# Kernel tuning notes

Hardware: AMD Instinct MI355X
Metric: run time of the kernel (lower is better)

## Reference

```python
import jax, jax.numpy as jnp
import numpy as np

N_NODES = 50000
N_EDGES = 600000
N_GRAPHS = 512
LN_EPS = 1e-5


def setup_inputs() -> dict:
    key = jax.random.key(0)
    ks = jax.random.split(key, 18)
    s = 0.05
    return {
        "x": jax.random.normal(ks[0], (N_NODES, 29), jnp.float32),
        "xdims": jax.random.normal(ks[1], (N_NODES, 3), jnp.float32),
        "xsttype": jax.random.randint(ks[2], (N_NODES,), 0, 256),
        "edge_index": jax.random.randint(ks[3], (2, N_EDGES), 0, N_NODES),
        "batch": jnp.sort(jax.random.randint(ks[4], (N_NODES,), 0, N_GRAPHS)),
        "st_emb": jax.random.normal(ks[5], (256, 12), jnp.float32) * s,
        "Wl1": jax.random.normal(ks[6], (128, 44), jnp.float32) * s,
        "bl1": jnp.zeros((128,), jnp.float32),
        "Wr1": jax.random.normal(ks[7], (128, 44), jnp.float32) * s,
        "g1": jnp.ones((128,), jnp.float32),
        "beta1": jnp.zeros((128,), jnp.float32),
        "Wl2": jax.random.normal(ks[8], (128, 128), jnp.float32) * s,
        "bl2": jnp.zeros((128,), jnp.float32),
        "Wr2": jax.random.normal(ks[9], (128, 128), jnp.float32) * s,
        "g2": jnp.ones((128,), jnp.float32),
        "beta2": jnp.zeros((128,), jnp.float32),
        "Wlin": jax.random.normal(ks[10], (10, 256), jnp.float32) * s,
        "blin": jnp.zeros((10,), jnp.float32),
    }


def layernorm(h, g, b):
    mu = jnp.mean(h, axis=-1, keepdims=True)
    var = jnp.mean(jnp.square(h - mu), axis=-1, keepdims=True)
    return g * (h - mu) * jax.lax.rsqrt(var + LN_EPS) + b


def sage_conv(h, src, dst, Wl, bl, Wr):
    # PyG SAGEConv: lin_l(mean_j x_j) + lin_r(x_i); messages flow src -> dst.
    msg = h[src]                                            # [E, D]
    agg = jax.ops.segment_sum(msg, dst, num_segments=N_NODES)
    cnt = jax.ops.segment_sum(jnp.ones((msg.shape[0],), h.dtype), dst, num_segments=N_NODES)
    mean = agg / jnp.maximum(cnt, 1.0)[:, None]
    return mean @ Wl.T + bl + h @ Wr.T


def reference(x, xdims, xsttype, edge_index, batch, st_emb,
              Wl1, bl1, Wr1, g1, beta1,
              Wl2, bl2, Wr2, g2, beta2,
              Wlin, blin):
    src, dst = edge_index[0], edge_index[1]
    h = jnp.concatenate([x, xdims, st_emb[xsttype]], axis=1)   # [N, 44]
    # Layer 1
    h = jax.nn.relu(layernorm(sage_conv(h, src, dst, Wl1, bl1, Wr1), g1, beta1))
    # Layer 2
    h = jax.nn.relu(layernorm(sage_conv(h, src, dst, Wl2, bl2, Wr2), g2, beta2))
    # dropout inactive (inference)
    hs = jax.ops.segment_sum(h, batch, num_segments=N_GRAPHS)
    nc = jax.ops.segment_sum(jnp.ones((h.shape[0],), h.dtype), batch, num_segments=N_GRAPHS)
    hmean = hs / jnp.maximum(nc, 1.0)[:, None]
    hmax = jax.ops.segment_max(h, batch, num_segments=N_GRAPHS)
    pooled = jnp.concatenate([hmean, hmax], axis=1)            # [G, 256]
    return pooled @ Wlin.T + blin                              # [G, 10]
```

## Files before the change

kernel.cpp:

```cpp
#include <hip/hip_runtime.h>
#include <hip/hip_bf16.h>
#include <math.h>

#define N_NODES 50000
#define N_EDGES 600000
#define N_GRAPHS 512
#define LN_EPS 1e-5f
#define CAP 96
#define EDGE_BLOCKS ((N_EDGES / 4 + 255) / 256)
#define PREP_BLOCKS ((N_NODES * 48 + 255) / 256)

typedef short bf16x8 __attribute__((ext_vector_type(8)));
typedef float f32x4 __attribute__((ext_vector_type(4)));

__device__ __forceinline__ unsigned short f2bf(float f) {
    unsigned int x = __float_as_uint(f);
    return (unsigned short)((x + 0x7fffu + ((x >> 16) & 1u)) >> 16);
}
__device__ __forceinline__ float bflo(unsigned int u) { return __uint_as_float(u << 16); }
__device__ __forceinline__ float bfhi(unsigned int u) { return __uint_as_float(u & 0xffff0000u); }

__global__ __launch_bounds__(256) void zero_kernel(int* __restrict__ cnt)
{
    int i = blockIdx.x * 256 + threadIdx.x;
    if (i < N_NODES) cnt[i] = 0;
}

__global__ __launch_bounds__(256) void prep_fill_kernel(
    const float* __restrict__ x, const float* __restrict__ xdims,
    const int* __restrict__ stt, const float* __restrict__ st_emb,
    const float* __restrict__ Wl1, const float* __restrict__ Wr1,
    const float* __restrict__ Wl2, const float* __restrict__ Wr2,
    const int* __restrict__ batch,
    const int* __restrict__ esrc_in, const int* __restrict__ edst_in,
    unsigned short* __restrict__ Xc1, unsigned short* __restrict__ Wc1,
    unsigned short* __restrict__ Wc2, int* __restrict__ cnt,
    int* __restrict__ esrc_pad, int* __restrict__ starts)
{
    if (blockIdx.x < EDGE_BLOCKS) {
        int t = blockIdx.x * 256 + threadIdx.x;
        int e4 = t * 4;
        if (e4 < N_EDGES) {
            int4 d4 = *(const int4*)(edst_in + e4);
            int4 s4 = *(const int4*)(esrc_in + e4);
            int sl0 = atomicAdd(&cnt[d4.x], 1);
            int sl1 = atomicAdd(&cnt[d4.y], 1);
            int sl2 = atomicAdd(&cnt[d4.z], 1);
            int sl3 = atomicAdd(&cnt[d4.w], 1);
            if (sl0 < CAP) esrc_pad[(size_t)d4.x * CAP + sl0] = s4.x;
            if (sl1 < CAP) esrc_pad[(size_t)d4.y * CAP + sl1] = s4.y;
            if (sl2 < CAP) esrc_pad[(size_t)d4.z * CAP + sl2] = s4.z;
            if (sl3 < CAP) esrc_pad[(size_t)d4.w * CAP + sl3] = s4.w;
        }
        return;
    }
    int idx = (blockIdx.x - EDGE_BLOCKS) * 256 + threadIdx.x;

    if (idx < N_NODES * 48) {
        int n = idx / 48;
        int c = idx - n * 48;
        float v;
        if (c < 29)       v = x[n * 29 + c];
        else if (c < 32)  v = xdims[n * 3 + (c - 29)];
        else if (c < 44)  v = st_emb[stt[n] * 12 + (c - 32)];
        else              v = 0.f;
        Xc1[(size_t)n * 96 + c] = f2bf(v);
    }
    if (idx < 128 * 96) {
        int f = idx / 96, k = idx - f * 96;
        float v;
        if (k < 44)       v = Wr1[f * 44 + k];
        else if (k < 48)  v = 0.f;
        else if (k < 92)  v = Wl1[f * 44 + (k - 48)];
        else              v = 0.f;
        Wc1[idx] = f2bf(v);
    }
    if (idx < 128 * 256) {
        int f = idx >> 8, k = idx & 255;
        float v = (k < 128) ? Wr2[f * 128 + k] : Wl2[f * 128 + (k - 128)];
        Wc2[idx] = f2bf(v);
    }
    if (idx < N_NODES) {
        int b = batch[idx];
        int pb = (idx == 0) ? -1 : batch[idx - 1];
        for (int g = pb + 1; g <= b; ++g) starts[g] = idx;
        if (idx == N_NODES - 1)
            for (int g = b + 1; g <= N_GRAPHS; ++g) starts[g] = N_NODES;
    }
}

__global__ __launch_bounds__(256) void agg1_kernel(const int* __restrict__ cnt,
                                                   const int* __restrict__ esrc_pad,
                                                   unsigned short* __restrict__ Xc)
{
    int n = blockIdx.x * 4 + (threadIdx.x >> 6);
    if (n >= N_NODES) return;
    const int lane = threadIdx.x & 63;
    const int grp = lane >> 3;
    const int sl  = lane & 7;
    const int slc = (sl < 5) ? sl : 5;
    int degT = cnt[n];
    int deg  = (degT < CAP) ? degT : CAP;
    int er = esrc_pad[(size_t)n * CAP + lane];
    float a0=0.f,a1=0.f,a2=0.f,a3=0.f,a4=0.f,a5=0.f,a6=0.f,a7=0.f;
    const uint4* base = (const uint4*)Xc;
    const int c1 = deg - 1;
    int lim = (deg < 64) ? deg : 64;
    for (int e = 0; e < lim; e += 16) {
        int eA = e + grp, eB = eA + 8;
        int sA = __shfl(er, (eA < c1) ? eA : c1);
        int sB = __shfl(er, (eB < c1) ? eB : c1);
        uint4 va = base[(size_t)sA * 12 + slc];
        uint4 vb = base[(size_t)sB * 12 + slc];
        float mA = (eA < deg) ? 1.f : 0.f;
        float mB = (eB < deg) ? 1.f : 0.f;
        a0 += mA * bflo(va.x) + mB * bflo(vb.x);
        a1 += mA * bfhi(va.x) + mB * bfhi(vb.x);
        a2 += mA * bflo(va.y) + mB * bflo(vb.y);
        a3 += mA * bfhi(va.y) + mB * bfhi(vb.y);
        a4 += mA * bflo(va.z) + mB * bflo(vb.z);
        a5 += mA * bfhi(va.z) + mB * bfhi(vb.z);
        a6 += mA * bflo(va.w) + mB * bflo(vb.w);
        a7 += mA * bfhi(va.w) + mB * bfhi(vb.w);
    }
    for (int e = 64; e < deg; e += 16) {
        int eA = e + grp, eB = eA + 8;
        int sA = esrc_pad[(size_t)n * CAP + ((eA < c1) ? eA : c1)];
        int sB = esrc_pad[(size_t)n * CAP + ((eB < c1) ? eB : c1)];
        uint4 va = base[(size_t)sA * 12 + slc];
        uint4 vb = base[(size_t)sB * 12 + slc];
        float mA = (eA < deg) ? 1.f : 0.f;
        float mB = (eB < deg) ? 1.f : 0.f;
        a0 += mA * bflo(va.x) + mB * bflo(vb.x);
        a1 += mA * bfhi(va.x) + mB * bfhi(vb.x);
        a2 += mA * bflo(va.y) + mB * bflo(vb.y);
        a3 += mA * bfhi(va.y) + mB * bfhi(vb.y);
        a4 += mA * bflo(va.z) + mB * bflo(vb.z);
        a5 += mA * bfhi(va.z) + mB * bfhi(vb.z);
        a6 += mA * bflo(va.w) + mB * bflo(vb.w);
        a7 += mA * bfhi(va.w) + mB * bfhi(vb.w);
    }
    #pragma unroll
    for (int m = 8; m <= 32; m <<= 1) {
        a0 += __shfl_xor(a0, m); a1 += __shfl_xor(a1, m);
        a2 += __shfl_xor(a2, m); a3 += __shfl_xor(a3, m);
        a4 += __shfl_xor(a4, m); a5 += __shfl_xor(a5, m);
        a6 += __shfl_xor(a6, m); a7 += __shfl_xor(a7, m);
    }
    if (grp == 0 && sl < 6) {
        float inv = (degT > 0) ? 1.f / (float)degT : 0.f;
        uint4 p;
        p.x = (unsigned int)f2bf(a0 * inv) | ((unsigned int)f2bf(a1 * inv) << 16);
        p.y = (unsigned int)f2bf(a2 * inv) | ((unsigned int)f2bf(a3 * inv) << 16);
        p.z = (unsigned int)f2bf(a4 * inv) | ((unsigned int)f2bf(a5 * inv) << 16);
        p.w = (unsigned int)f2bf(a6 * inv) | ((unsigned int)f2bf(a7 * inv) << 16);
        ((uint4*)Xc)[(size_t)n * 12 + 6 + sl] = p;
    }
}

__global__ __launch_bounds__(256) void agg2_kernel(const int* __restrict__ cnt,
                                                   const int* __restrict__ esrc_pad,
                                                   unsigned short* __restrict__ Xc)
{
    int n = blockIdx.x * 4 + (threadIdx.x >> 6);
    if (n >= N_NODES) return;
    const int lane = threadIdx.x & 63;
    const int grp = lane >> 4;
    const int sl  = lane & 15;
    int degT = cnt[n];
    int deg  = (degT < CAP) ? degT : CAP;
    int er = esrc_pad[(size_t)n * CAP + lane];
    float a0=0.f,a1=0.f,a2=0.f,a3=0.f,a4=0.f,a5=0.f,a6=0.f,a7=0.f;
    const uint4* base = (const uint4*)Xc;
    const int c1 = deg - 1;
    int lim = (deg < 64) ? deg : 64;
    for (int e = 0; e < lim; e += 16) {
        int eA = e + grp, eB = eA + 4, eC = eA + 8, eD = eA + 12;
        int sA = __shfl(er, (eA < c1) ? eA : c1);
        int sB = __shfl(er, (eB < c1) ? eB : c1);
        int sC = __shfl(er, (eC < c1) ? eC : c1);
        int sD = __shfl(er, (eD < c1) ? eD : c1);
        uint4 va = base[(size_t)sA * 32 + sl];
        uint4 vb = base[(size_t)sB * 32 + sl];
        uint4 vc = base[(size_t)sC * 32 + sl];
        uint4 vd = base[(size_t)sD * 32 + sl];
        float mA = (eA < deg) ? 1.f : 0.f;
        float mB = (eB < deg) ? 1.f : 0.f;
        float mC = (eC < deg) ? 1.f : 0.f;
        float mD = (eD < deg) ? 1.f : 0.f;
        a0 += mA * bflo(va.x) + mB * bflo(vb.x) + mC * bflo(vc.x) + mD * bflo(vd.x);
        a1 += mA * bfhi(va.x) + mB * bfhi(vb.x) + mC * bfhi(vc.x) + mD * bfhi(vd.x);
        a2 += mA * bflo(va.y) + mB * bflo(vb.y) + mC * bflo(vc.y) + mD * bflo(vd.y);
        a3 += mA * bfhi(va.y) + mB * bfhi(vb.y) + mC * bfhi(vc.y) + mD * bfhi(vd.y);
        a4 += mA * bflo(va.z) + mB * bflo(vb.z) + mC * bflo(vc.z) + mD * bflo(vd.z);
        a5 += mA * bfhi(va.z) + mB * bfhi(vb.z) + mC * bfhi(vc.z) + mD * bfhi(vd.z);
        a6 += mA * bflo(va.w) + mB * bflo(vb.w) + mC * bflo(vc.w) + mD * bflo(vd.w);
        a7 += mA * bfhi(va.w) + mB * bfhi(vb.w) + mC * bfhi(vc.w) + mD * bfhi(vd.w);
    }
    for (int e = 64; e < deg; e += 16) {
        int eA = e + grp, eB = eA + 4, eC = eA + 8, eD = eA + 12;
        int sA = esrc_pad[(size_t)n * CAP + ((eA < c1) ? eA : c1)];
        int sB = esrc_pad[(size_t)n * CAP + ((eB < c1) ? eB : c1)];
        int sC = esrc_pad[(size_t)n * CAP + ((eC < c1) ? eC : c1)];
        int sD = esrc_pad[(size_t)n * CAP + ((eD < c1) ? eD : c1)];
        uint4 va = base[(size_t)sA * 32 + sl];
        uint4 vb = base[(size_t)sB * 32 + sl];
        uint4 vc = base[(size_t)sC * 32 + sl];
        uint4 vd = base[(size_t)sD * 32 + sl];
        float mA = (eA < deg) ? 1.f : 0.f;
        float mB = (eB < deg) ? 1.f : 0.f;
        float mC = (eC < deg) ? 1.f : 0.f;
        float mD = (eD < deg) ? 1.f : 0.f;
        a0 += mA * bflo(va.x) + mB * bflo(vb.x) + mC * bflo(vc.x) + mD * bflo(vd.x);
        a1 += mA * bfhi(va.x) + mB * bfhi(vb.x) + mC * bfhi(vc.x) + mD * bfhi(vd.x);
        a2 += mA * bflo(va.y) + mB * bflo(vb.y) + mC * bflo(vc.y) + mD * bflo(vd.y);
        a3 += mA * bfhi(va.y) + mB * bfhi(vb.y) + mC * bfhi(vc.y) + mD * bfhi(vd.y);
        a4 += mA * bflo(va.z) + mB * bflo(vb.z) + mC * bflo(vc.z) + mD * bflo(vd.z);
        a5 += mA * bfhi(va.z) + mB * bfhi(vb.z) + mC * bfhi(vc.z) + mD * bfhi(vd.z);
        a6 += mA * bflo(va.w) + mB * bflo(vb.w) + mC * bflo(vc.w) + mD * bflo(vd.w);
        a7 += mA * bfhi(va.w) + mB * bfhi(vb.w) + mC * bfhi(vc.w) + mD * bfhi(vd.w);
    }
    #pragma unroll
    for (int m = 16; m <= 32; m <<= 1) {
        a0 += __shfl_xor(a0, m); a1 += __shfl_xor(a1, m);
        a2 += __shfl_xor(a2, m); a3 += __shfl_xor(a3, m);
        a4 += __shfl_xor(a4, m); a5 += __shfl_xor(a5, m);
        a6 += __shfl_xor(a6, m); a7 += __shfl_xor(a7, m);
    }
    if (grp == 0) {
        float inv = (degT > 0) ? 1.f / (float)degT : 0.f;
        uint4 p;
        p.x = (unsigned int)f2bf(a0 * inv) | ((unsigned int)f2bf(a1 * inv) << 16);
        p.y = (unsigned int)f2bf(a2 * inv) | ((unsigned int)f2bf(a3 * inv) << 16);
        p.z = (unsigned int)f2bf(a4 * inv) | ((unsigned int)f2bf(a5 * inv) << 16);
        p.w = (unsigned int)f2bf(a6 * inv) | ((unsigned int)f2bf(a7 * inv) << 16);
        ((uint4*)Xc)[(size_t)n * 32 + 16 + sl] = p;
    }
}

template <int KPAD>
__global__ __launch_bounds__(256) void mfma_layer_kernel(
    const unsigned short* __restrict__ X, const unsigned short* __restrict__ W,
    const float* __restrict__ bl, const float* __restrict__ g,
    const float* __restrict__ beta,
    unsigned short* __restrict__ Out, int outStride)
{
    const int lane = threadIdx.x & 63;
    const int wv   = threadIdx.x >> 6;
    const int l15  = lane & 15;
    const int l4   = lane >> 4;
    const int row0 = blockIdx.x * 128 + wv * 32;

    int rA0 = row0 + l15;       if (rA0 > N_NODES - 1) rA0 = N_NODES - 1;
    int rA1 = row0 + 16 + l15;  if (rA1 > N_NODES - 1) rA1 = N_NODES - 1;

    f32x4 acc[2][8];
    #pragma unroll
    for (int m = 0; m < 2; ++m)
        #pragma unroll
        for (int n = 0; n < 8; ++n) acc[m][n] = (f32x4){0.f, 0.f, 0.f, 0.f};

    const int kb = l4 * 8;
    #pragma unroll
    for (int ks = 0; ks < KPAD / 32; ++ks) {
        const int k = ks * 32 + kb;
        bf16x8 a0 = *(const bf16x8*)(X + (size_t)rA0 * KPAD + k);
        bf16x8 a1 = *(const bf16x8*)(X + (size_t)rA1 * KPAD + k);
        #pragma unroll
        for (int ni = 0; ni < 8; ++ni) {
            bf16x8 b = *(const bf16x8*)(W + (size_t)(ni * 16 + l15) * KPAD + k);
            acc[0][ni] = __builtin_amdgcn_mfma_f32_16x16x32_bf16(a0, b, acc[0][ni], 0, 0, 0);
            acc[1][ni] = __builtin_amdgcn_mfma_f32_16x16x32_bf16(a1, b, acc[1][ni], 0, 0, 0);
        }
    }

    float blv[8], gv[8], bev[8];
    #pragma unroll
    for (int ni = 0; ni < 8; ++ni) {
        int f = ni * 16 + l15;
        blv[ni] = bl[f]; gv[ni] = g[f]; bev[ni] = beta[f];
    }

    #pragma unroll
    for (int mi = 0; mi < 2; ++mi) {
        #pragma unroll
        for (int r = 0; r < 4; ++r) {
            float v[8];
            float s1 = 0.f, s2 = 0.f;
            #pragma unroll
            for (int ni = 0; ni < 8; ++ni) {
                float t = acc[mi][ni][r] + blv[ni];
                v[ni] = t; s1 += t; s2 += t * t;
            }
            #pragma unroll
            for (int m = 8; m >= 1; m >>= 1) {
                s1 += __shfl_xor(s1, m);
                s2 += __shfl_xor(s2, m);
            }
            float mu   = s1 * (1.f / 128.f);
            float var  = s2 * (1.f / 128.f) - mu * mu;
            float rstd = rsqrtf(var + LN_EPS);
            int node = row0 + mi * 16 + l4 * 4 + r;
            if (node < N_NODES) {
                #pragma unroll
                for (int ni = 0; ni < 8; ++ni) {
                    float o = gv[ni] * (v[ni] - mu) * rstd + bev[ni];
                    o = fmaxf(o, 0.f);
                    Out[(size_t)node * outStride + ni * 16 + l15] = f2bf(o);
                }
            }
        }
    }
}

__global__ __launch_bounds__(256) void poolhead_kernel(const unsigned short* __restrict__ h2,
                                                       const int* __restrict__ starts,
                                                       const float* __restrict__ Wlin,
                                                       const float* __restrict__ blin,
                                                       float* __restrict__ out)
{
    const int g  = blockIdx.x;
    const int j2 = threadIdx.x & 63;
    const int h  = threadIdx.x >> 6;
    const int s0 = starts[g], s1 = starts[g + 1];
    float sa = 0.f, sb = 0.f, ma = -INFINITY, mb = -INFINITY;
    const unsigned int* base = (const unsigned int*)h2;
    int n = s0 + h;
    for (; n + 4 < s1; n += 8) {
        unsigned int u0 = base[(size_t)n * 64 + j2];
        unsigned int u1 = base[(size_t)(n + 4) * 64 + j2];
        float l0 = bflo(u0), h0 = bfhi(u0);
        float l1 = bflo(u1), h1 = bfhi(u1);
        sa += l0 + l1; sb += h0 + h1;
        ma = fmaxf(ma, fmaxf(l0, l1));
        mb = fmaxf(mb, fmaxf(h0, h1));
    }
    if (n < s1) {
        unsigned int u = base[(size_t)n * 64 + j2];
        float lo = bflo(u), hi = bfhi(u);
        sa += lo; sb += hi;
        ma = fmaxf(ma, lo); mb = fmaxf(mb, hi);
    }
    __shared__ float red[4][4][64];
    __shared__ float pooled[256];
    red[h][0][j2] = sa; red[h][1][j2] = sb; red[h][2][j2] = ma; red[h][3][j2] = mb;
    __syncthreads();
    if (h == 0) {
        #pragma unroll
        for (int o = 1; o < 4; ++o) {
            sa += red[o][0][j2]; sb += red[o][1][j2];
            ma = fmaxf(ma, red[o][2][j2]); mb = fmaxf(mb, red[o][3][j2]);
        }
        int c = s1 - s0;
        float inv = (c > 0) ? 1.f / (float)c : 0.f;
        pooled[2 * j2]           = sa * inv;
        pooled[2 * j2 + 1]       = sb * inv;
        pooled[128 + 2 * j2]     = (c > 0) ? ma : 0.f;
        pooled[128 + 2 * j2 + 1] = (c > 0) ? mb : 0.f;
    }
    __syncthreads();
    if (threadIdx.x < 10) {
        const float* w = Wlin + threadIdx.x * 256;
        float acc = blin[threadIdx.x];
        for (int k = 0; k < 256; ++k) acc += pooled[k] * w[k];
        out[g * 10 + threadIdx.x] = acc;
    }
}

extern "C" void kernel_launch(void* const* d_in, const int* in_sizes, int n_in,
                              void* d_out, int out_size, void* d_ws, size_t ws_size,
                              hipStream_t stream)
{
    const float* x      = (const float*)d_in[0];
    const float* xdims  = (const float*)d_in[1];
    const int*   stt    = (const int*)d_in[2];
    const int*   eidx   = (const int*)d_in[3];
    const int*   batch  = (const int*)d_in[4];
    const float* st_emb = (const float*)d_in[5];
    const float* Wl1 = (const float*)d_in[6];
    const float* bl1 = (const float*)d_in[7];
    const float* Wr1 = (const float*)d_in[8];
    const float* g1  = (const float*)d_in[9];
    const float* be1 = (const float*)d_in[10];
    const float* Wl2 = (const float*)d_in[11];
    const float* bl2 = (const float*)d_in[12];
    const float* Wr2 = (const float*)d_in[13];
    const float* g2  = (const float*)d_in[14];
    const float* be2 = (const float*)d_in[15];
    const float* Wlin = (const float*)d_in[16];
    const float* blin = (const float*)d_in[17];
    float* out = (float*)d_out;

    const int* esrc_in = eidx;
    const int* edst_in = eidx + N_EDGES;

    char* ws = (char*)d_ws;
    size_t o = 0;
    auto carve = [&](size_t bytes) { void* p = ws + o; o = (o + bytes + 255) & ~(size_t)255; return p; };
    unsigned short* Xc1  = (unsigned short*)carve((size_t)N_NODES * 96 * 2);
    unsigned short* Xc2  = (unsigned short*)carve((size_t)N_NODES * 256 * 2);
    unsigned short* h2bf = (unsigned short*)carve((size_t)N_NODES * 128 * 2);
    unsigned short* Wc1  = (unsigned short*)carve((size_t)128 * 96 * 2);
    unsigned short* Wc2  = (unsigned short*)carve((size_t)128 * 256 * 2);
    int*   cnt      = (int*)carve((size_t)N_NODES * 4);
    int*   esrc_pad = (int*)carve((size_t)N_NODES * CAP * 4);
    int*   starts   = (int*)carve((size_t)(N_GRAPHS + 1) * 4);
    (void)ws_size;

    zero_kernel<<<(N_NODES + 255) / 256, 256, 0, stream>>>(cnt);

    prep_fill_kernel<<<EDGE_BLOCKS + PREP_BLOCKS, 256, 0, stream>>>(
        x, xdims, stt, st_emb, Wl1, Wr1, Wl2, Wr2, batch,
        esrc_in, edst_in, Xc1, Wc1, Wc2, cnt, esrc_pad, starts);

    agg1_kernel<<<(N_NODES + 3) / 4, 256, 0, stream>>>(cnt, esrc_pad, Xc1);
    mfma_layer_kernel<96><<<(N_NODES + 127) / 128, 256, 0, stream>>>(
        Xc1, Wc1, bl1, g1, be1, Xc2, 256);

    agg2_kernel<<<(N_NODES + 3) / 4, 256, 0, stream>>>(cnt, esrc_pad, Xc2);
    mfma_layer_kernel<256><<<(N_NODES + 127) / 128, 256, 0, stream>>>(
        Xc2, Wc2, bl2, g2, be2, h2bf, 128);

    poolhead_kernel<<<N_GRAPHS, 256, 0, stream>>>(h2bf, starts, Wlin, blin, out);
}
```

Measured before the change: 130.8 us.

## Fuse neighbor mean aggregation into MFMA layer kernels with 16-bit adjacency

Each layer's separate gather-mean kernel is removed. Each wave now aggregates neighbor features for its 16 nodes into LDS, then runs the MFMA GEMM with LayerNorm and ReLU, reading the self half from global memory and the mean half from shared memory. This drops two launches and the global write and re-read of the aggregated features. The adjacency list shrinks to 16-bit indices with a 64-slot cap, and node feature buffers hold only the self half. In exchange, each wave aggregates its 16 nodes one after another, which may hide gather latency less well, and any node with more than 64 in-edges has the extra edges dropped from its sum.

```diff
diff --git a/kernel.cpp b/kernel.cpp
--- a/kernel.cpp
+++ b/kernel.cpp
@@ -6,9 +6,9 @@
 #define N_EDGES 600000
 #define N_GRAPHS 512
 #define LN_EPS 1e-5f
-#define CAP 96
+#define CAP 64
 #define EDGE_BLOCKS ((N_EDGES / 4 + 255) / 256)
-#define PREP_BLOCKS ((N_NODES * 48 + 255) / 256)
+#define PREP_BLOCKS ((N_NODES * 64 + 255) / 256)
 
 typedef short bf16x8 __attribute__((ext_vector_type(8)));
 typedef float f32x4 __attribute__((ext_vector_type(4)));
@@ -33,9 +33,9 @@
     const float* __restrict__ Wl2, const float* __restrict__ Wr2,
     const int* __restrict__ batch,
     const int* __restrict__ esrc_in, const int* __restrict__ edst_in,
-    unsigned short* __restrict__ Xc1, unsigned short* __restrict__ Wc1,
+    unsigned short* __restrict__ Xh1, unsigned short* __restrict__ Wc1,
     unsigned short* __restrict__ Wc2, int* __restrict__ cnt,
-    int* __restrict__ esrc_pad, int* __restrict__ starts)
+    unsigned short* __restrict__ adj, int* __restrict__ starts)
 {
     if (blockIdx.x < EDGE_BLOCKS) {
         int t = blockIdx.x * 256 + threadIdx.x;
@@ -47,32 +47,32 @@
             int sl1 = atomicAdd(&cnt[d4.y], 1);
             int sl2 = atomicAdd(&cnt[d4.z], 1);
             int sl3 = atomicAdd(&cnt[d4.w], 1);
-            if (sl0 < CAP) esrc_pad[(size_t)d4.x * CAP + sl0] = s4.x;
-            if (sl1 < CAP) esrc_pad[(size_t)d4.y * CAP + sl1] = s4.y;
-            if (sl2 < CAP) esrc_pad[(size_t)d4.z * CAP + sl2] = s4.z;
-            if (sl3 < CAP) esrc_pad[(size_t)d4.w * CAP + sl3] = s4.w;
+            if (sl0 < CAP) adj[(size_t)d4.x * CAP + sl0] = (unsigned short)s4.x;
+            if (sl1 < CAP) adj[(size_t)d4.y * CAP + sl1] = (unsigned short)s4.y;
+            if (sl2 < CAP) adj[(size_t)d4.z * CAP + sl2] = (unsigned short)s4.z;
+            if (sl3 < CAP) adj[(size_t)d4.w * CAP + sl3] = (unsigned short)s4.w;
         }
         return;
     }
     int idx = (blockIdx.x - EDGE_BLOCKS) * 256 + threadIdx.x;
 
-    if (idx < N_NODES * 48) {
-        int n = idx / 48;
-        int c = idx - n * 48;
+    if (idx < N_NODES * 64) {
+        int n = idx >> 6;
+        int c = idx & 63;
         float v;
         if (c < 29)       v = x[n * 29 + c];
         else if (c < 32)  v = xdims[n * 3 + (c - 29)];
         else if (c < 44)  v = st_emb[stt[n] * 12 + (c - 32)];
         else              v = 0.f;
-        Xc1[(size_t)n * 96 + c] = f2bf(v);
-    }
-    if (idx < 128 * 96) {
-        int f = idx / 96, k = idx - f * 96;
+        Xh1[idx] = f2bf(v);
+    }
+    if (idx < 128 * 128) {
+        int f = idx >> 7, k = idx & 127;
         float v;
-        if (k < 44)       v = Wr1[f * 44 + k];
-        else if (k < 48)  v = 0.f;
-        else if (k < 92)  v = Wl1[f * 44 + (k - 48)];
-        else              v = 0.f;
+        if (k < 44)        v = Wr1[f * 44 + k];
+        else if (k < 64)   v = 0.f;
+        else if (k < 108)  v = Wl1[f * 44 + (k - 64)];
+        else               v = 0.f;
         Wc1[idx] = f2bf(v);
     }
     if (idx < 128 * 256) {
@@ -89,188 +89,97 @@
     }
 }
 
-__global__ __launch_bounds__(256) void agg1_kernel(const int* __restrict__ cnt,
-                                                   const int* __restrict__ esrc_pad,
-                                                   unsigned short* __restrict__ Xc)
-{
-    int n = blockIdx.x * 4 + (threadIdx.x >> 6);
-    if (n >= N_NODES) return;
-    const int lane = threadIdx.x & 63;
-    const int grp = lane >> 3;
-    const int sl  = lane & 7;
-    const int slc = (sl < 5) ? sl : 5;
-    int degT = cnt[n];
-    int deg  = (degT < CAP) ? degT : CAP;
-    int er = esrc_pad[(size_t)n * CAP + lane];
-    float a0=0.f,a1=0.f,a2=0.f,a3=0.f,a4=0.f,a5=0.f,a6=0.f,a7=0.f;
-    const uint4* base = (const uint4*)Xc;
-    const int c1 = deg - 1;
-    int lim = (deg < 64) ? deg : 64;
-    for (int e = 0; e < lim; e += 16) {
-        int eA = e + grp, eB = eA + 8;
-        int sA = __shfl(er, (eA < c1) ? eA : c1);
-        int sB = __shfl(er, (eB < c1) ? eB : c1);
-        uint4 va = base[(size_t)sA * 12 + slc];
-        uint4 vb = base[(size_t)sB * 12 + slc];
-        float mA = (eA < deg) ? 1.f : 0.f;
-        float mB = (eB < deg) ? 1.f : 0.f;
-        a0 += mA * bflo(va.x) + mB * bflo(vb.x);
-        a1 += mA * bfhi(va.x) + mB * bfhi(vb.x);
-        a2 += mA * bflo(va.y) + mB * bflo(vb.y);
-        a3 += mA * bfhi(va.y) + mB * bfhi(vb.y);
-        a4 += mA * bflo(va.z) + mB * bflo(vb.z);
-        a5 += mA * bfhi(va.z) + mB * bfhi(vb.z);
-        a6 += mA * bflo(va.w) + mB * bflo(vb.w);
-        a7 += mA * bfhi(va.w) + mB * bfhi(vb.w);
-    }
-    for (int e = 64; e < deg; e += 16) {
-        int eA = e + grp, eB = eA + 8;
-        int sA = esrc_pad[(size_t)n * CAP + ((eA < c1) ? eA : c1)];
-        int sB = esrc_pad[(size_t)n * CAP + ((eB < c1) ? eB : c1)];
-        uint4 va = base[(size_t)sA * 12 + slc];
-        uint4 vb = base[(size_t)sB * 12 + slc];
-        float mA = (eA < deg) ? 1.f : 0.f;
-        float mB = (eB < deg) ? 1.f : 0.f;
-        a0 += mA * bflo(va.x) + mB * bflo(vb.x);
-        a1 += mA * bfhi(va.x) + mB * bfhi(vb.x);
-        a2 += mA * bflo(va.y) + mB * bflo(vb.y);
-        a3 += mA * bfhi(va.y) + mB * bfhi(vb.y);
-        a4 += mA * bflo(va.z) + mB * bflo(vb.z);
-        a5 += mA * bfhi(va.z) + mB * bfhi(vb.z);
-        a6 += mA * bflo(va.w) + mB * bflo(vb.w);
-        a7 += mA * bfhi(va.w) + mB * bfhi(vb.w);
-    }
-    #pragma unroll
-    for (int m = 8; m <= 32; m <<= 1) {
-        a0 += __shfl_xor(a0, m); a1 += __shfl_xor(a1, m);
-        a2 += __shfl_xor(a2, m); a3 += __shfl_xor(a3, m);
-        a4 += __shfl_xor(a4, m); a5 += __shfl_xor(a5, m);
-        a6 += __shfl_xor(a6, m); a7 += __shfl_xor(a7, m);
-    }
-    if (grp == 0 && sl < 6) {
-        float inv = (degT > 0) ? 1.f / (float)degT : 0.f;
-        uint4 p;
-        p.x = (unsigned int)f2bf(a0 * inv) | ((unsigned int)f2bf(a1 * inv) << 16);
-        p.y = (unsigned int)f2bf(a2 * inv) | ((unsigned int)f2bf(a3 * inv) << 16);
-        p.z = (unsigned int)f2bf(a4 * inv) | ((unsigned int)f2bf(a5 * inv) << 16);
-        p.w = (unsigned int)f2bf(a6 * inv) | ((unsigned int)f2bf(a7 * inv) << 16);
-        ((uint4*)Xc)[(size_t)n * 12 + 6 + sl] = p;
-    }
-}
-
-__global__ __launch_bounds__(256) void agg2_kernel(const int* __restrict__ cnt,
-                                                   const int* __restrict__ esrc_pad,
-                                                   unsigned short* __restrict__ Xc)
-{
-    int n = blockIdx.x * 4 + (threadIdx.x >> 6);
-    if (n >= N_NODES) return;
-    const int lane = threadIdx.x & 63;
-    const int grp = lane >> 4;
-    const int sl  = lane & 15;
-    int degT = cnt[n];
-    int deg  = (degT < CAP) ? degT : CAP;
-    int er = esrc_pad[(size_t)n * CAP + lane];
-    float a0=0.f,a1=0.f,a2=0.f,a3=0.f,a4=0.f,a5=0.f,a6=0.f,a7=0.f;
-    const uint4* base = (const uint4*)Xc;
-    const int c1 = deg - 1;
-    int lim = (deg < 64) ? deg : 64;
-    for (int e = 0; e < lim; e += 16) {
-        int eA = e + grp, eB = eA + 4, eC = eA + 8, eD = eA + 12;
-        int sA = __shfl(er, (eA < c1) ? eA : c1);
-        int sB = __shfl(er, (eB < c1) ? eB : c1);
-        int sC = __shfl(er, (eC < c1) ? eC : c1);
-        int sD = __shfl(er, (eD < c1) ? eD : c1);
-        uint4 va = base[(size_t)sA * 32 + sl];
-        uint4 vb = base[(size_t)sB * 32 + sl];
-        uint4 vc = base[(size_t)sC * 32 + sl];
-        uint4 vd = base[(size_t)sD * 32 + sl];
-        float mA = (eA < deg) ? 1.f : 0.f;
-        float mB = (eB < deg) ? 1.f : 0.f;
-        float mC = (eC < deg) ? 1.f : 0.f;
-        float mD = (eD < deg) ? 1.f : 0.f;
-        a0 += mA * bflo(va.x) + mB * bflo(vb.x) + mC * bflo(vc.x) + mD * bflo(vd.x);
-        a1 += mA * bfhi(va.x) + mB * bfhi(vb.x) + mC * bfhi(vc.x) + mD * bfhi(vd.x);
-        a2 += mA * bflo(va.y) + mB * bflo(vb.y) + mC * bflo(vc.y) + mD * bflo(vd.y);
-        a3 += mA * bfhi(va.y) + mB * bfhi(vb.y) + mC * bfhi(vc.y) + mD * bfhi(vd.y);
-        a4 += mA * bflo(va.z) + mB * bflo(vb.z) + mC * bflo(vc.z) + mD * bflo(vd.z);
-        a5 += mA * bfhi(va.z) + mB * bfhi(vb.z) + mC * bfhi(vc.z) + mD * bfhi(vd.z);
-        a6 += mA * bflo(va.w) + mB * bflo(vb.w) + mC * bflo(vc.w) + mD * bflo(vd.w);
-        a7 += mA * bfhi(va.w) + mB * bfhi(vb.w) + mC * bfhi(vc.w) + mD * bfhi(vd.w);
-    }
-    for (int e = 64; e < deg; e += 16) {
-        int eA = e + grp, eB = eA + 4, eC = eA + 8, eD = eA + 12;
-        int sA = esrc_pad[(size_t)n * CAP + ((eA < c1) ? eA : c1)];
-        int sB = esrc_pad[(size_t)n * CAP + ((eB < c1) ? eB : c1)];
-        int sC = esrc_pad[(size_t)n * CAP + ((eC < c1) ? eC : c1)];
-        int sD = esrc_pad[(size_t)n * CAP + ((eD < c1) ? eD : c1)];
-        uint4 va = base[(size_t)sA * 32 + sl];
-        uint4 vb = base[(size_t)sB * 32 + sl];
-        uint4 vc = base[(size_t)sC * 32 + sl];
-        uint4 vd = base[(size_t)sD * 32 + sl];
-        float mA = (eA < deg) ? 1.f : 0.f;
-        float mB = (eB < deg) ? 1.f : 0.f;
-        float mC = (eC < deg) ? 1.f : 0.f;
-        float mD = (eD < deg) ? 1.f : 0.f;
-        a0 += mA * bflo(va.x) + mB * bflo(vb.x) + mC * bflo(vc.x) + mD * bflo(vd.x);
-        a1 += mA * bfhi(va.x) + mB * bfhi(vb.x) + mC * bfhi(vc.x) + mD * bfhi(vd.x);
-        a2 += mA * bflo(va.y) + mB * bflo(vb.y) + mC * bflo(vc.y) + mD * bflo(vd.y);
-        a3 += mA * bfhi(va.y) + mB * bfhi(vb.y) + mC * bfhi(vc.y) + mD * bfhi(vd.y);
-        a4 += mA * bflo(va.z) + mB * bflo(vb.z) + mC * bflo(vc.z) + mD * bflo(vd.z);
-        a5 += mA * bfhi(va.z) + mB * bfhi(vb.z) + mC * bfhi(vc.z) + mD * bfhi(vd.z);
-        a6 += mA * bflo(va.w) + mB * bflo(vb.w) + mC * bflo(vc.w) + mD * bflo(vd.w);
-        a7 += mA * bfhi(va.w) + mB * bfhi(vb.w) + mC * bfhi(vc.w) + mD * bfhi(vd.w);
-    }
-    #pragma unroll
-    for (int m = 16; m <= 32; m <<= 1) {
-        a0 += __shfl_xor(a0, m); a1 += __shfl_xor(a1, m);
-        a2 += __shfl_xor(a2, m); a3 += __shfl_xor(a3, m);
-        a4 += __shfl_xor(a4, m); a5 += __shfl_xor(a5, m);
-        a6 += __shfl_xor(a6, m); a7 += __shfl_xor(a7, m);
-    }
-    if (grp == 0) {
-        float inv = (degT > 0) ? 1.f / (float)degT : 0.f;
-        uint4 p;
-        p.x = (unsigned int)f2bf(a0 * inv) | ((unsigned int)f2bf(a1 * inv) << 16);
-        p.y = (unsigned int)f2bf(a2 * inv) | ((unsigned int)f2bf(a3 * inv) << 16);
-        p.z = (unsigned int)f2bf(a4 * inv) | ((unsigned int)f2bf(a5 * inv) << 16);
-        p.w = (unsigned int)f2bf(a6 * inv) | ((unsigned int)f2bf(a7 * inv) << 16);
-        ((uint4*)Xc)[(size_t)n * 32 + 16 + sl] = p;
-    }
-}
-
 template <int KPAD>
-__global__ __launch_bounds__(256) void mfma_layer_kernel(
-    const unsigned short* __restrict__ X, const unsigned short* __restrict__ W,
+__global__ __launch_bounds__(256) void fused_layer_kernel(
+    const int* __restrict__ cnt, const unsigned short* __restrict__ adj,
+    const unsigned short* __restrict__ Xh,
+    const unsigned short* __restrict__ W,
     const float* __restrict__ bl, const float* __restrict__ g,
     const float* __restrict__ beta,
-    unsigned short* __restrict__ Out, int outStride)
-{
-    const int lane = threadIdx.x & 63;
-    const int wv   = threadIdx.x >> 6;
-    const int l15  = lane & 15;
-    const int l4   = lane >> 4;
-    const int row0 = blockIdx.x * 128 + wv * 32;
-
-    int rA0 = row0 + l15;       if (rA0 > N_NODES - 1) rA0 = N_NODES - 1;
-    int rA1 = row0 + 16 + l15;  if (rA1 > N_NODES - 1) rA1 = N_NODES - 1;
-
-    f32x4 acc[2][8];
+    unsigned short* __restrict__ Out)
+{
+    constexpr int DHALF = KPAD / 2;
+    constexpr int CH  = DHALF / 8;
+    constexpr int NG  = 64 / CH;
+    constexpr int NL  = 16 / NG;
+    constexpr int RSU = CH + 1;
+    __shared__ uint4 smean[64 * RSU];
+
+    const int lane  = threadIdx.x & 63;
+    const int wv    = threadIdx.x >> 6;
+    const int nbase = blockIdx.x * 64 + wv * 16;
+
+    {
+        const int grp = lane / CH;
+        const int sl  = lane % CH;
+        const uint4* gbase = (const uint4*)Xh;
+        for (int i = 0; i < 16; ++i) {
+            int n = nbase + i;
+            if (n >= N_NODES) break;
+            int degT = cnt[n];
+            int deg  = (degT < CAP) ? degT : CAP;
+            int er = adj[(size_t)n * CAP + lane];
+            float a0=0.f,a1=0.f,a2=0.f,a3=0.f,a4=0.f,a5=0.f,a6=0.f,a7=0.f;
+            const int c1 = deg - 1;
+            for (int e = 0; e < deg; e += 16) {
+                uint4 v[NL]; float mk[NL];
+                #pragma unroll
+                for (int j = 0; j < NL; ++j) {
+                    int ee = e + j * NG + grp;
+                    int s = __shfl(er, (ee < c1) ? ee : c1);
+                    v[j]  = gbase[(size_t)s * CH + sl];
+                    mk[j] = (ee < deg) ? 1.f : 0.f;
+                }
+                #pragma unroll
+                for (int j = 0; j < NL; ++j) {
+                    a0 += mk[j] * bflo(v[j].x); a1 += mk[j] * bfhi(v[j].x);
+                    a2 += mk[j] * bflo(v[j].y); a3 += mk[j] * bfhi(v[j].y);
+                    a4 += mk[j] * bflo(v[j].z); a5 += mk[j] * bfhi(v[j].z);
+                    a6 += mk[j] * bflo(v[j].w); a7 += mk[j] * bfhi(v[j].w);
+                }
+            }
+            #pragma unroll
+            for (int m = CH; m <= 32; m <<= 1) {
+                a0 += __shfl_xor(a0, m); a1 += __shfl_xor(a1, m);
+                a2 += __shfl_xor(a2, m); a3 += __shfl_xor(a3, m);
+                a4 += __shfl_xor(a4, m); a5 += __shfl_xor(a5, m);
+                a6 += __shfl_xor(a6, m); a7 += __shfl_xor(a7, m);
+            }
+            if (grp == 0) {
+                float inv = (degT > 0) ? 1.f / (float)degT : 0.f;
+                uint4 p;
+                p.x = (unsigned int)f2bf(a0 * inv) | ((unsigned int)f2bf(a1 * inv) << 16);
+                p.y = (unsigned int)f2bf(a2 * inv) | ((unsigned int)f2bf(a3 * inv) << 16);
+                p.z = (unsigned int)f2bf(a4 * inv) | ((unsigned int)f2bf(a5 * inv) << 16);
+                p.w = (unsigned int)f2bf(a6 * inv) | ((unsigned int)f2bf(a7 * inv) << 16);
+                smean[(size_t)(wv * 16 + i) * RSU + sl] = p;
+            }
+        }
+    }
+
+    const int l15 = lane & 15;
+    const int l4  = lane >> 4;
+    int rA = nbase + l15; if (rA > N_NODES - 1) rA = N_NODES - 1;
+
+    f32x4 acc[8];
     #pragma unroll
-    for (int m = 0; m < 2; ++m)
-        #pragma unroll
-        for (int n = 0; n < 8; ++n) acc[m][n] = (f32x4){0.f, 0.f, 0.f, 0.f};
+    for (int n = 0; n < 8; ++n) acc[n] = (f32x4){0.f, 0.f, 0.f, 0.f};
 
     const int kb = l4 * 8;
+    const unsigned short* sm = (const unsigned short*)smean;
     #pragma unroll
     for (int ks = 0; ks < KPAD / 32; ++ks) {
         const int k = ks * 32 + kb;
-        bf16x8 a0 = *(const bf16x8*)(X + (size_t)rA0 * KPAD + k);
-        bf16x8 a1 = *(const bf16x8*)(X + (size_t)rA1 * KPAD + k);
+        bf16x8 a;
+        if (ks < KPAD / 64) {
+            a = *(const bf16x8*)(Xh + (size_t)rA * DHALF + k);
+        } else {
+            a = *(const bf16x8*)(sm + (size_t)(wv * 16 + l15) * RSU * 8 + (k - DHALF));
+        }
         #pragma unroll
         for (int ni = 0; ni < 8; ++ni) {
             bf16x8 b = *(const bf16x8*)(W + (size_t)(ni * 16 + l15) * KPAD + k);
-            acc[0][ni] = __builtin_amdgcn_mfma_f32_16x16x32_bf16(a0, b, acc[0][ni], 0, 0, 0);
-            acc[1][ni] = __builtin_amdgcn_mfma_f32_16x16x32_bf16(a1, b, acc[1][ni], 0, 0, 0);
+            acc[ni] = __builtin_amdgcn_mfma_f32_16x16x32_bf16(a, b, acc[ni], 0, 0, 0);
         }
     }
 
@@ -282,32 +191,29 @@
     }
 
     #pragma unroll
-    for (int mi = 0; mi < 2; ++mi) {
+    for (int r = 0; r < 4; ++r) {
+        float v[8];
+        float s1 = 0.f, s2 = 0.f;
         #pragma unroll
-        for (int r = 0; r < 4; ++r) {
-            float v[8];
-            float s1 = 0.f, s2 = 0.f;
+        for (int ni = 0; ni < 8; ++ni) {
+            float t = acc[ni][r] + blv[ni];
+            v[ni] = t; s1 += t; s2 += t * t;
+        }
+        #pragma unroll
+        for (int m = 8; m >= 1; m >>= 1) {
+            s1 += __shfl_xor(s1, m);
+            s2 += __shfl_xor(s2, m);
+        }
+        float mu   = s1 * (1.f / 128.f);
+        float var  = s2 * (1.f / 128.f) - mu * mu;
+        float rstd = rsqrtf(var + LN_EPS);
+        int node = nbase + l4 * 4 + r;
+        if (node < N_NODES) {
             #pragma unroll
             for (int ni = 0; ni < 8; ++ni) {
-                float t = acc[mi][ni][r] + blv[ni];
-                v[ni] = t; s1 += t; s2 += t * t;
-            }
-            #pragma unroll
-            for (int m = 8; m >= 1; m >>= 1) {
-                s1 += __shfl_xor(s1, m);
-                s2 += __shfl_xor(s2, m);
-            }
-            float mu   = s1 * (1.f / 128.f);
-            float var  = s2 * (1.f / 128.f) - mu * mu;
-            float rstd = rsqrtf(var + LN_EPS);
-            int node = row0 + mi * 16 + l4 * 4 + r;
-            if (node < N_NODES) {
-                #pragma unroll
-                for (int ni = 0; ni < 8; ++ni) {
-                    float o = gv[ni] * (v[ni] - mu) * rstd + bev[ni];
-                    o = fmaxf(o, 0.f);
-                    Out[(size_t)node * outStride + ni * 16 + l15] = f2bf(o);
-                }
+                float o = gv[ni] * (v[ni] - mu) * rstd + bev[ni];
+                o = fmaxf(o, 0.f);
+                Out[(size_t)node * 128 + ni * 16 + l15] = f2bf(o);
             }
         }
     }
@@ -397,29 +303,27 @@
     char* ws = (char*)d_ws;
     size_t o = 0;
     auto carve = [&](size_t bytes) { void* p = ws + o; o = (o + bytes + 255) & ~(size_t)255; return p; };
-    unsigned short* Xc1  = (unsigned short*)carve((size_t)N_NODES * 96 * 2);
-    unsigned short* Xc2  = (unsigned short*)carve((size_t)N_NODES * 256 * 2);
+    unsigned short* Xh1  = (unsigned short*)carve((size_t)N_NODES * 64 * 2);
+    unsigned short* Xh2  = (unsigned short*)carve((size_t)N_NODES * 128 * 2);
     unsigned short* h2bf = (unsigned short*)carve((size_t)N_NODES * 128 * 2);
-    unsigned short* Wc1  = (unsigned short*)carve((size_t)128 * 96 * 2);
+    unsigned short* Wc1  = (unsigned short*)carve((size_t)128 * 128 * 2);
     unsigned short* Wc2  = (unsigned short*)carve((size_t)128 * 256 * 2);
-    int*   cnt      = (int*)carve((size_t)N_NODES * 4);
-    int*   esrc_pad = (int*)carve((size_t)N_NODES * CAP * 4);
-    int*   starts   = (int*)carve((size_t)(N_GRAPHS + 1) * 4);
+    int*            cnt  = (int*)carve((size_t)N_NODES * 4);
+    unsigned short* adj  = (unsigned short*)carve((size_t)N_NODES * CAP * 2);
+    int*          starts = (int*)carve((size_t)(N_GRAPHS + 1) * 4);
     (void)ws_size;
 
     zero_kernel<<<(N_NODES + 255) / 256, 256, 0, stream>>>(cnt);
 
     prep_fill_kernel<<<EDGE_BLOCKS + PREP_BLOCKS, 256, 0, stream>>>(
         x, xdims, stt, st_emb, Wl1, Wr1, Wl2, Wr2, batch,
-        esrc_in, edst_in, Xc1, Wc1, Wc2, cnt, esrc_pad, starts);
-
-    agg1_kernel<<<(N_NODES + 3) / 4, 256, 0, stream>>>(cnt, esrc_pad, Xc1);
-    mfma_layer_kernel<96><<<(N_NODES + 127) / 128, 256, 0, stream>>>(
-        Xc1, Wc1, bl1, g1, be1, Xc2, 256);
-
-    agg2_kernel<<<(N_NODES + 3) / 4, 256, 0, stream>>>(cnt, esrc_pad, Xc2);
-    mfma_layer_kernel<256><<<(N_NODES + 127) / 128, 256, 0, stream>>>(
-        Xc2, Wc2, bl2, g2, be2, h2bf, 128);
+        esrc_in, edst_in, Xh1, Wc1, Wc2, cnt, adj, starts);
+
+    fused_layer_kernel<128><<<(N_NODES + 63) / 64, 256, 0, stream>>>(
+        cnt, adj, Xh1, Wc1, bl1, g1, be1, Xh2);
+
+    fused_layer_kernel<256><<<(N_NODES + 63) / 64, 256, 0, stream>>>(
+        cnt, adj, Xh2, Wc2, bl2, g2, be2, h2bf);
 
     poolhead_kernel<<<N_GRAPHS, 256, 0, stream>>>(h2bf, starts, Wlin, blin, out);
 }
```

Result: slower. 156.9 us (+20.0%).
